# Kernel tuning notes

Hardware: AMD Instinct MI355X
Metric: run time of the kernel (lower is better)

Reference implementation:

```python
import jax, jax.numpy as jnp
import numpy as np

GROUP = 16  # quantization group size along in_features
EPS = 1e-5


def _qlora_linear(x, qw, sc, b, la, lb):
    # qw: [O, I] int4 codes; sc: [O, I//GROUP] fp32 group scales
    O, I = qw.shape
    w = (qw.astype(jnp.float32).reshape(O, I // GROUP, GROUP) * sc[:, :, None]).reshape(O, I)
    base = x @ w.T + b                      # [N, O]
    lora = (x @ la.T) @ lb.T                # [N, R] @ [R, O]
    return base + lora


def _layernorm(x, g, b):
    m = jnp.mean(x, axis=-1, keepdims=True)
    v = jnp.var(x, axis=-1, keepdims=True)
    return (x - m) * jax.lax.rsqrt(v + EPS) * g + b


def setup_inputs() -> dict:
    key = jax.random.key(0)
    ks = jax.random.split(key, 8)
    N, D, R, L = 16384, 1024, 32, 18  # tokens, BIGNET_DIM, lora_dim, num linears
    x = jax.random.normal(ks[0], (N, D), jnp.float32)
    qw = jax.random.randint(ks[1], (L, D, D), -8, 8, jnp.int32)  # signed 4-bit codes
    scales = jax.random.uniform(ks[2], (L, D, D // GROUP), jnp.float32, 0.005, 0.02)
    bias = 0.01 * jax.random.normal(ks[3], (L, D), jnp.float32)
    la = 0.001 * jax.random.normal(ks[4], (L, R, D), jnp.float32)
    lb = 0.01 * jax.random.normal(ks[5], (L, D, R), jnp.float32)
    ln_g = jnp.ones((5, D), jnp.float32) + 0.1 * jax.random.normal(ks[6], (5, D), jnp.float32)
    ln_b = 0.01 * jax.random.normal(ks[7], (5, D), jnp.float32)
    return {"x": x, "qw": qw, "scales": scales, "bias": bias,
            "la": la, "lb": lb, "ln_g": ln_g, "ln_b": ln_b}


def reference(x, qw, scales, bias, la, lb, ln_g, ln_b):
    h = x
    for blk in range(6):
        y = h
        for j in range(3):
            i = blk * 3 + j
            y = _qlora_linear(y, qw[i], scales[i], bias[i], la[i], lb[i])
            if j < 2:
                y = jax.nn.relu(y)
        h = y + h  # residual
        if blk < 5:
            h = _layernorm(h, ln_g[blk], ln_b[blk])
    return h
```

## Files before the change

### kernel.cpp

```cpp
#include <hip/hip_runtime.h>

#define DIM 1024
#define NTOK 16384

typedef __attribute__((ext_vector_type(8))) _Float16 f16x8;
typedef __attribute__((ext_vector_type(4))) _Float16 f16x4;
typedef __attribute__((ext_vector_type(4))) float f32x4;

__device__ __forceinline__ void gload_lds16(const void* g, void* l) {
  __builtin_amdgcn_global_load_lds(
      (const __attribute__((address_space(1))) void*)g,
      (__attribute__((address_space(3))) void*)l, 16, 0, 0);
}

__device__ __forceinline__ f16x8 ldsr(const char* smem, int byteoff) {
  return *(const f16x8*)(smem + byteoff);
}

__device__ __forceinline__ f32x4 mfma16(f16x8 a, f16x8 b, f32x4 c) {
  return __builtin_amdgcn_mfma_f32_16x16x32_f16(a, b, c, 0, 0, 0);
}

__global__ __launch_bounds__(256) void cvt_kernel(const float* __restrict__ in,
                                                  _Float16* __restrict__ out) {
  const int i = blockIdx.x * 256 + threadIdx.x;
  float4 v = reinterpret_cast<const float4*>(in)[i];
  f16x4 o;
  o[0] = (_Float16)v.x;
  o[1] = (_Float16)v.y;
  o[2] = (_Float16)v.z;
  o[3] = (_Float16)v.w;
  *reinterpret_cast<f16x4*>(&out[(size_t)i * 4]) = o;
}

__global__ __launch_bounds__(256) void build_weff(const int* __restrict__ qw,
                                                  const float* __restrict__ scales,
                                                  const float* __restrict__ la,
                                                  const float* __restrict__ lb,
                                                  _Float16* __restrict__ W) {
  __shared__ float la_s[32][256];
  __shared__ float lb_s[32][32];
  const int kt = blockIdx.x;
  const int ot = blockIdx.y;
  const int l = blockIdx.z;
  const int tid = threadIdx.x;

  for (int idx = tid; idx < 2048; idx += 256) {
    const int r = idx >> 6, c4 = (idx & 63) * 4;
    *(float4*)&la_s[r][c4] =
        *(const float4*)&la[((size_t)l * 32 + r) * DIM + kt * 256 + c4];
  }
  {
    const int o = tid >> 3, r4 = (tid & 7) * 4;
    *(float4*)&lb_s[o][r4] =
        *(const float4*)&lb[((size_t)l * DIM + ot * 32 + o) * 32 + r4];
  }
  __syncthreads();

  const int kq = tid & 63;
  const int os = tid >> 6;
  const int k0 = kq * 4;
  const int kg = kt * 256 + k0;
  const size_t rb = (size_t)l * DIM + ot * 32 + os * 8;

  int4 q[8];
  float sc[8];
#pragma unroll
  for (int oi = 0; oi < 8; ++oi) {
    q[oi] = *(const int4*)&qw[(rb + oi) * DIM + kg];
    sc[oi] = scales[(rb + oi) * 64 + (kg >> 4)];
  }

  float acc[8][4];
#pragma unroll
  for (int a = 0; a < 8; ++a)
#pragma unroll
    for (int b = 0; b < 4; ++b) acc[a][b] = 0.f;

#pragma unroll
  for (int r4 = 0; r4 < 8; ++r4) {
    float lbr[8][4];
#pragma unroll
    for (int oi = 0; oi < 8; ++oi) {
      const float4 v = *(const float4*)&lb_s[os * 8 + oi][r4 * 4];
      lbr[oi][0] = v.x;
      lbr[oi][1] = v.y;
      lbr[oi][2] = v.z;
      lbr[oi][3] = v.w;
    }
#pragma unroll
    for (int rr = 0; rr < 4; ++rr) {
      const float4 a4 = *(const float4*)&la_s[r4 * 4 + rr][k0];
#pragma unroll
      for (int oi = 0; oi < 8; ++oi) {
        acc[oi][0] = fmaf(lbr[oi][rr], a4.x, acc[oi][0]);
        acc[oi][1] = fmaf(lbr[oi][rr], a4.y, acc[oi][1]);
        acc[oi][2] = fmaf(lbr[oi][rr], a4.z, acc[oi][2]);
        acc[oi][3] = fmaf(lbr[oi][rr], a4.w, acc[oi][3]);
      }
    }
  }

#pragma unroll
  for (int oi = 0; oi < 8; ++oi) {
    f16x4 o4;
    o4[0] = (_Float16)(fmaf((float)q[oi].x, sc[oi], acc[oi][0]));
    o4[1] = (_Float16)(fmaf((float)q[oi].y, sc[oi], acc[oi][1]));
    o4[2] = (_Float16)(fmaf((float)q[oi].z, sc[oi], acc[oi][2]));
    o4[3] = (_Float16)(fmaf((float)q[oi].w, sc[oi], acc[oi][3]));
    *(f16x4*)&W[(rb + oi) * DIM + kg] = o4;
  }
}

#define ST_NONE ((void)0)
#define VM_NONE ((void)0)
#define VM4 asm volatile("s_waitcnt vmcnt(4)" ::: "memory")
#define VM0 asm volatile("s_waitcnt vmcnt(0)" ::: "memory")

#define RDA(BUF, FM, KS) \
  ldsr(smem, (((BUF)*2 + wm) << 14) + (((FM)*16 + r16) << 7) + (cks ^ ((KS) << 6)))
#define RDB(BUF, FN, KS)                                                        \
  ldsr(smem, 65536 + (((BUF)*2 + (wn >> 1)) << 14) +                            \
                 ((((wn & 1) * 64) + (FN)*16 + r16) << 7) + (cks ^ ((KS) << 6)))

#define PH(QQ, BUFC, STAGE, VMASM)                                          \
  {                                                                         \
    if ((QQ) == 0) {                                                        \
      _Pragma("unroll") for (int fn = 0; fn < 4; ++fn) {                    \
        bf[fn][0] = RDB(BUFC, fn, 0);                                       \
        bf[fn][1] = RDB(BUFC, fn, 1);                                       \
      }                                                                     \
    }                                                                       \
    f16x8 a00 = RDA(BUFC, 2 * (QQ), 0);                                     \
    f16x8 a01 = RDA(BUFC, 2 * (QQ), 1);                                     \
    f16x8 a10 = RDA(BUFC, 2 * (QQ) + 1, 0);                                 \
    f16x8 a11 = RDA(BUFC, 2 * (QQ) + 1, 1);                                 \
    STAGE;                                                                  \
    asm volatile("" ::: "memory");                                          \
    __builtin_amdgcn_s_barrier();                                           \
    asm volatile("s_waitcnt lgkmcnt(0)" ::: "memory");                      \
    __builtin_amdgcn_s_setprio(1);                                          \
    _Pragma("unroll") for (int fn = 0; fn < 4; ++fn) {                      \
      acc[2 * (QQ)][fn] = mfma16(bf[fn][0], a00, acc[2 * (QQ)][fn]);        \
      acc[2 * (QQ)][fn] = mfma16(bf[fn][1], a01, acc[2 * (QQ)][fn]);        \
      acc[2 * (QQ) + 1][fn] = mfma16(bf[fn][0], a10, acc[2 * (QQ) + 1][fn]); \
      acc[2 * (QQ) + 1][fn] = mfma16(bf[fn][1], a11, acc[2 * (QQ) + 1][fn]); \
    }                                                                       \
    __builtin_amdgcn_s_setprio(0);                                          \
    VMASM;                                                                  \
    asm volatile("" ::: "memory");                                          \
    __builtin_amdgcn_s_barrier();                                           \
  }

template <int MODE>
__global__ __launch_bounds__(512, 2) void qgemm(const _Float16* __restrict__ X,
                                                const _Float16* __restrict__ W,
                                                const float* __restrict__ bias,
                                                const _Float16* __restrict__ RES,
                                                void* __restrict__ OUT) {
  extern __shared__ char smem[];

  const int tid = threadIdx.x;
  const int wave = tid >> 6;
  const int lane = tid & 63;
  const int wm = wave >> 2;
  const int wn = wave & 3;
  const int bn = blockIdx.x;
  const int bm = blockIdx.y;

  const int r16 = lane & 15;
  const int cks = ((lane >> 4) * 16) ^ ((lane & 7) << 4);

  const int srl = lane >> 3;
  const int scs = ((lane & 7) ^ srl) << 3;

  f32x4 acc[8][4];
#pragma unroll
  for (int i = 0; i < 8; ++i)
#pragma unroll
    for (int j = 0; j < 4; ++j)
#pragma unroll
      for (int r = 0; r < 4; ++r) acc[i][j][r] = 0.f;

  auto stageA = [&](int buf, int h, int t) {
    const _Float16* g =
        X + (size_t)(bm * 256 + h * 128 + wave * 16 + srl) * DIM + t * 64 + scs;
    char* d = smem + (((buf * 2 + h) << 14) + wave * 2048);
    gload_lds16(g, d);
    gload_lds16(g + 8 * DIM, d + 1024);
  };
  auto stageB = [&](int buf, int h, int t) {
    const _Float16* g =
        W + (size_t)(bn * 256 + h * 128 + wave * 16 + srl) * DIM + t * 64 + scs;
    char* d = smem + (65536 + ((buf * 2 + h) << 14) + wave * 2048);
    gload_lds16(g, d);
    gload_lds16(g + 8 * DIM, d + 1024);
  };

  stageA(0, 0, 0);
  stageA(0, 1, 0);
  stageB(0, 0, 0);
  stageB(0, 1, 0);
  stageB(1, 0, 1);
  stageB(1, 1, 1);
  VM4;
  __builtin_amdgcn_s_barrier();

  f16x8 bf[4][2];

  for (int i = 0; i < 7; ++i) {
    const int t0 = 2 * i, t1 = 2 * i + 1;
    PH(0, 0, stageA(1, 0, t1), VM_NONE)
    PH(1, 0, stageA(1, 1, t1), VM_NONE)
    PH(2, 0, stageB(0, 0, t0 + 2), VM_NONE)
    PH(3, 0, stageB(0, 1, t0 + 2), VM4)
    PH(0, 1, stageA(0, 0, t0 + 2), VM_NONE)
    PH(1, 1, stageA(0, 1, t0 + 2), VM_NONE)
    PH(2, 1, stageB(1, 0, t1 + 2), VM_NONE)
    PH(3, 1, stageB(1, 1, t1 + 2), VM4)
  }
  PH(0, 0, stageA(1, 0, 15), VM_NONE)
  PH(1, 0, stageA(1, 1, 15), VM_NONE)
  PH(2, 0, ST_NONE, VM_NONE)
  PH(3, 0, ST_NONE, VM0)
  PH(0, 1, ST_NONE, VM_NONE)
  PH(1, 1, ST_NONE, VM_NONE)
  PH(2, 1, ST_NONE, VM_NONE)
  PH(3, 1, ST_NONE, VM_NONE)

  const int m_base = bm * 256 + wm * 128 + r16;
  const int o_base = bn * 256 + wn * 64 + (lane >> 4) * 4;
  float4 bv4[4];
#pragma unroll
  for (int fn = 0; fn < 4; ++fn)
    bv4[fn] = *(const float4*)&bias[o_base + fn * 16];

#pragma unroll
  for (int fm = 0; fm < 8; ++fm) {
    const size_t rowoff = (size_t)(m_base + fm * 16) * DIM;
#pragma unroll
    for (int fn = 0; fn < 4; ++fn) {
      const int o = o_base + fn * 16;
      float v0 = acc[fm][fn][0] + bv4[fn].x;
      float v1 = acc[fm][fn][1] + bv4[fn].y;
      float v2 = acc[fm][fn][2] + bv4[fn].z;
      float v3 = acc[fm][fn][3] + bv4[fn].w;
      if (MODE == 0) {
        f16x4 s;
        s[0] = (_Float16)fmaxf(v0, 0.f);
        s[1] = (_Float16)fmaxf(v1, 0.f);
        s[2] = (_Float16)fmaxf(v2, 0.f);
        s[3] = (_Float16)fmaxf(v3, 0.f);
        *(f16x4*)&((_Float16*)OUT)[rowoff + o] = s;
      } else {
        const f16x4 rv = *(const f16x4*)&RES[rowoff + o];
        v0 += (float)rv[0];
        v1 += (float)rv[1];
        v2 += (float)rv[2];
        v3 += (float)rv[3];
        if (MODE == 1) {
          f16x4 s;
          s[0] = (_Float16)v0;
          s[1] = (_Float16)v1;
          s[2] = (_Float16)v2;
          s[3] = (_Float16)v3;
          *(f16x4*)&((_Float16*)OUT)[rowoff + o] = s;
        } else {
          float4 s = {v0, v1, v2, v3};
          *(float4*)&((float*)OUT)[rowoff + o] = s;
        }
      }
    }
  }
}

__global__ __launch_bounds__(256) void ln_kernel(const _Float16* __restrict__ in,
                                                 const float* __restrict__ g,
                                                 const float* __restrict__ b,
                                                 _Float16* __restrict__ out) {
  const int row = blockIdx.x;
  const int tid = threadIdx.x;
  const _Float16* rp = in + (size_t)row * DIM;

  f16x4 raw = reinterpret_cast<const f16x4*>(rp)[tid];
  float v0 = (float)raw[0], v1 = (float)raw[1], v2 = (float)raw[2], v3 = (float)raw[3];
  float s = v0 + v1 + v2 + v3;
  float sq = v0 * v0 + v1 * v1 + v2 * v2 + v3 * v3;
#pragma unroll
  for (int off = 32; off > 0; off >>= 1) {
    s += __shfl_down(s, off);
    sq += __shfl_down(sq, off);
  }
  __shared__ float ss[4], sq4[4];
  if ((tid & 63) == 0) {
    ss[tid >> 6] = s;
    sq4[tid >> 6] = sq;
  }
  __syncthreads();
  s = ss[0] + ss[1] + ss[2] + ss[3];
  sq = sq4[0] + sq4[1] + sq4[2] + sq4[3];
  const float mean = s * (1.f / DIM);
  const float var = sq * (1.f / DIM) - mean * mean;
  const float inv = rsqrtf(var + 1e-5f);

  float4 gv = reinterpret_cast<const float4*>(g)[tid];
  float4 bv = reinterpret_cast<const float4*>(b)[tid];
  f16x4 o;
  o[0] = (_Float16)((v0 - mean) * inv * gv.x + bv.x);
  o[1] = (_Float16)((v1 - mean) * inv * gv.y + bv.y);
  o[2] = (_Float16)((v2 - mean) * inv * gv.z + bv.z);
  o[3] = (_Float16)((v3 - mean) * inv * gv.w + bv.w);
  *reinterpret_cast<f16x4*>(&out[(size_t)row * DIM + tid * 4]) = o;
}


extern "C" void kernel_launch(void* const* d_in, const int* in_sizes, int n_in,
                              void* d_out, int out_size, void* d_ws, size_t ws_size,
                              hipStream_t stream) {
  const float* x = (const float*)d_in[0];
  const int* qw = (const int*)d_in[1];
  const float* scales = (const float*)d_in[2];
  const float* bias = (const float*)d_in[3];
  const float* la = (const float*)d_in[4];
  const float* lb = (const float*)d_in[5];
  const float* ln_g = (const float*)d_in[6];
  const float* ln_b = (const float*)d_in[7];

  char* ws = (char*)d_ws;
  const size_t WEFF_BYTES = (size_t)18 * DIM * DIM * 2;
  const size_t ACT_BYTES = (size_t)NTOK * DIM * 2;
  _Float16* Weff = (_Float16*)ws;
  _Float16* bufA = (_Float16*)(ws + WEFF_BYTES);
  _Float16* bufB = (_Float16*)(ws + WEFF_BYTES + ACT_BYTES);
  _Float16* bufC = (_Float16*)(ws + WEFF_BYTES + 2 * ACT_BYTES);

  const int LDS_BYTES = 131072;
  (void)hipFuncSetAttribute((const void*)&qgemm<0>,
                            hipFuncAttributeMaxDynamicSharedMemorySize, LDS_BYTES);
  (void)hipFuncSetAttribute((const void*)&qgemm<1>,
                            hipFuncAttributeMaxDynamicSharedMemorySize, LDS_BYTES);
  (void)hipFuncSetAttribute((const void*)&qgemm<2>,
                            hipFuncAttributeMaxDynamicSharedMemorySize, LDS_BYTES);

  cvt_kernel<<<NTOK * DIM / 1024, 256, 0, stream>>>(x, bufA);
  build_weff<<<dim3(4, 32, 18), 256, 0, stream>>>(qw, scales, la, lb, Weff);

  const dim3 ggrid(DIM / 256, NTOK / 256);
  for (int blk = 0; blk < 6; ++blk) {
    const int i0 = blk * 3;
    const size_t wstep = (size_t)DIM * DIM;
    qgemm<0><<<ggrid, 512, LDS_BYTES, stream>>>(bufA, Weff + (size_t)i0 * wstep,
                                                bias + i0 * DIM, nullptr, bufB);
    qgemm<0><<<ggrid, 512, LDS_BYTES, stream>>>(bufB, Weff + (size_t)(i0 + 1) * wstep,
                                                bias + (i0 + 1) * DIM, nullptr, bufC);
    if (blk < 5) {
      qgemm<1><<<ggrid, 512, LDS_BYTES, stream>>>(bufC, Weff + (size_t)(i0 + 2) * wstep,
                                                  bias + (i0 + 2) * DIM, bufA, bufB);
      ln_kernel<<<NTOK, 256, 0, stream>>>(bufB, ln_g + blk * DIM, ln_b + blk * DIM, bufA);
    } else {
      qgemm<2><<<ggrid, 512, LDS_BYTES, stream>>>(bufC, Weff + (size_t)(i0 + 2) * wstep,
                                                  bias + (i0 + 2) * DIM, bufA, d_out);
    }
  }
}
```

Measured before the change: 869.8 us.

## Load weight fragments directly to registers, stage only activations through LDS

```diff
diff --git a/kernel.cpp b/kernel.cpp
--- a/kernel.cpp
+++ b/kernel.cpp
@@ -112,53 +112,13 @@
   }
 }
 
-#define ST_NONE ((void)0)
-#define VM_NONE ((void)0)
-#define VM4 asm volatile("s_waitcnt vmcnt(4)" ::: "memory")
-#define VM0 asm volatile("s_waitcnt vmcnt(0)" ::: "memory")
-
-#define RDA(BUF, FM, KS) \
-  ldsr(smem, (((BUF)*2 + wm) << 14) + (((FM)*16 + r16) << 7) + (cks ^ ((KS) << 6)))
-#define RDB(BUF, FN, KS)                                                        \
-  ldsr(smem, 65536 + (((BUF)*2 + (wn >> 1)) << 14) +                            \
-                 ((((wn & 1) * 64) + (FN)*16 + r16) << 7) + (cks ^ ((KS) << 6)))
-
-#define PH(QQ, BUFC, STAGE, VMASM)                                          \
-  {                                                                         \
-    if ((QQ) == 0) {                                                        \
-      _Pragma("unroll") for (int fn = 0; fn < 4; ++fn) {                    \
-        bf[fn][0] = RDB(BUFC, fn, 0);                                       \
-        bf[fn][1] = RDB(BUFC, fn, 1);                                       \
-      }                                                                     \
-    }                                                                       \
-    f16x8 a00 = RDA(BUFC, 2 * (QQ), 0);                                     \
-    f16x8 a01 = RDA(BUFC, 2 * (QQ), 1);                                     \
-    f16x8 a10 = RDA(BUFC, 2 * (QQ) + 1, 0);                                 \
-    f16x8 a11 = RDA(BUFC, 2 * (QQ) + 1, 1);                                 \
-    STAGE;                                                                  \
-    asm volatile("" ::: "memory");                                          \
-    __builtin_amdgcn_s_barrier();                                           \
-    asm volatile("s_waitcnt lgkmcnt(0)" ::: "memory");                      \
-    __builtin_amdgcn_s_setprio(1);                                          \
-    _Pragma("unroll") for (int fn = 0; fn < 4; ++fn) {                      \
-      acc[2 * (QQ)][fn] = mfma16(bf[fn][0], a00, acc[2 * (QQ)][fn]);        \
-      acc[2 * (QQ)][fn] = mfma16(bf[fn][1], a01, acc[2 * (QQ)][fn]);        \
-      acc[2 * (QQ) + 1][fn] = mfma16(bf[fn][0], a10, acc[2 * (QQ) + 1][fn]); \
-      acc[2 * (QQ) + 1][fn] = mfma16(bf[fn][1], a11, acc[2 * (QQ) + 1][fn]); \
-    }                                                                       \
-    __builtin_amdgcn_s_setprio(0);                                          \
-    VMASM;                                                                  \
-    asm volatile("" ::: "memory");                                          \
-    __builtin_amdgcn_s_barrier();                                           \
-  }
-
 template <int MODE>
 __global__ __launch_bounds__(512, 2) void qgemm(const _Float16* __restrict__ X,
                                                 const _Float16* __restrict__ W,
                                                 const float* __restrict__ bias,
                                                 const _Float16* __restrict__ RES,
                                                 void* __restrict__ OUT) {
-  extern __shared__ char smem[];
+  __shared__ char smem[65536];
 
   const int tid = threadIdx.x;
   const int wave = tid >> 6;
@@ -169,7 +129,8 @@
   const int bm = blockIdx.y;
 
   const int r16 = lane & 15;
-  const int cks = ((lane >> 4) * 16) ^ ((lane & 7) << 4);
+  const int koff = lane >> 4;
+  const int cks = (koff * 16) ^ ((lane & 7) << 4);
 
   const int srl = lane >> 3;
   const int scs = ((lane & 7) ^ srl) << 3;
@@ -182,58 +143,68 @@
 #pragma unroll
       for (int r = 0; r < 4; ++r) acc[i][j][r] = 0.f;
 
-  auto stageA = [&](int buf, int h, int t) {
+  auto stageA = [&](int buf, int t) {
     const _Float16* g =
-        X + (size_t)(bm * 256 + h * 128 + wave * 16 + srl) * DIM + t * 64 + scs;
-    char* d = smem + (((buf * 2 + h) << 14) + wave * 2048);
+        X + (size_t)(bm * 256 + wave * 16 + srl) * DIM + t * 64 + scs;
+    char* d = smem + (buf << 15) + wave * 2048;
     gload_lds16(g, d);
     gload_lds16(g + 8 * DIM, d + 1024);
+    gload_lds16(g + 128 * DIM, d + 16384);
+    gload_lds16(g + 136 * DIM, d + 16384 + 1024);
   };
-  auto stageB = [&](int buf, int h, int t) {
-    const _Float16* g =
-        W + (size_t)(bn * 256 + h * 128 + wave * 16 + srl) * DIM + t * 64 + scs;
-    char* d = smem + (65536 + ((buf * 2 + h) << 14) + wave * 2048);
-    gload_lds16(g, d);
-    gload_lds16(g + 8 * DIM, d + 1024);
+
+  const _Float16* Wb = W + (size_t)(bn * 256 + wn * 64 + r16) * DIM + koff * 8;
+  auto loadB = [&](f16x8(&b)[4][2], int t) {
+#pragma unroll
+    for (int fn = 0; fn < 4; ++fn)
+#pragma unroll
+      for (int ks = 0; ks < 2; ++ks)
+        b[fn][ks] = *(const f16x8*)(Wb + (size_t)fn * 16 * DIM + t * 64 + ks * 32);
   };
 
-  stageA(0, 0, 0);
-  stageA(0, 1, 0);
-  stageB(0, 0, 0);
-  stageB(0, 1, 0);
-  stageB(1, 0, 1);
-  stageB(1, 1, 1);
-  VM4;
-  __builtin_amdgcn_s_barrier();
-
-  f16x8 bf[4][2];
-
-  for (int i = 0; i < 7; ++i) {
-    const int t0 = 2 * i, t1 = 2 * i + 1;
-    PH(0, 0, stageA(1, 0, t1), VM_NONE)
-    PH(1, 0, stageA(1, 1, t1), VM_NONE)
-    PH(2, 0, stageB(0, 0, t0 + 2), VM_NONE)
-    PH(3, 0, stageB(0, 1, t0 + 2), VM4)
-    PH(0, 1, stageA(0, 0, t0 + 2), VM_NONE)
-    PH(1, 1, stageA(0, 1, t0 + 2), VM_NONE)
-    PH(2, 1, stageB(1, 0, t1 + 2), VM_NONE)
-    PH(3, 1, stageB(1, 1, t1 + 2), VM4)
-  }
-  PH(0, 0, stageA(1, 0, 15), VM_NONE)
-  PH(1, 0, stageA(1, 1, 15), VM_NONE)
-  PH(2, 0, ST_NONE, VM_NONE)
-  PH(3, 0, ST_NONE, VM0)
-  PH(0, 1, ST_NONE, VM_NONE)
-  PH(1, 1, ST_NONE, VM_NONE)
-  PH(2, 1, ST_NONE, VM_NONE)
-  PH(3, 1, ST_NONE, VM_NONE)
+  f16x8 b0[4][2], b1[4][2];
+
+  stageA(0, 0);
+  loadB(b0, 0);
+
+#define TILE(T, BCUR, BNEXT)                                                 \
+  {                                                                          \
+    asm volatile("s_waitcnt vmcnt(0)" ::: "memory");                         \
+    __builtin_amdgcn_s_barrier();                                            \
+    if ((T) + 1 < 16) {                                                      \
+      stageA(((T) + 1) & 1, (T) + 1);                                        \
+      loadB(BNEXT, (T) + 1);                                                 \
+    }                                                                        \
+    const int bufo = ((T)&1) << 15;                                          \
+    __builtin_amdgcn_s_setprio(1);                                           \
+    _Pragma("unroll") for (int q = 0; q < 4; ++q) {                          \
+      const int ra0 = bufo + ((wm * 128 + (2 * q) * 16 + r16) << 7);         \
+      const int ra1 = bufo + ((wm * 128 + (2 * q + 1) * 16 + r16) << 7);     \
+      f16x8 a00 = ldsr(smem, ra0 + cks);                                     \
+      f16x8 a01 = ldsr(smem, ra0 + (cks ^ 64));                              \
+      f16x8 a10 = ldsr(smem, ra1 + cks);                                     \
+      f16x8 a11 = ldsr(smem, ra1 + (cks ^ 64));                              \
+      _Pragma("unroll") for (int fn = 0; fn < 4; ++fn) {                     \
+        acc[2 * q][fn] = mfma16(BCUR[fn][0], a00, acc[2 * q][fn]);           \
+        acc[2 * q][fn] = mfma16(BCUR[fn][1], a01, acc[2 * q][fn]);           \
+        acc[2 * q + 1][fn] = mfma16(BCUR[fn][0], a10, acc[2 * q + 1][fn]);   \
+        acc[2 * q + 1][fn] = mfma16(BCUR[fn][1], a11, acc[2 * q + 1][fn]);   \
+      }                                                                      \
+    }                                                                        \
+    __builtin_amdgcn_s_setprio(0);                                           \
+  }
+
+  for (int t = 0; t < 16; t += 2) {
+    TILE(t, b0, b1)
+    TILE(t + 1, b1, b0)
+  }
+#undef TILE
 
   const int m_base = bm * 256 + wm * 128 + r16;
   const int o_base = bn * 256 + wn * 64 + (lane >> 4) * 4;
   float4 bv4[4];
 #pragma unroll
-  for (int fn = 0; fn < 4; ++fn)
-    bv4[fn] = *(const float4*)&bias[o_base + fn * 16];
+  for (int fn = 0; fn < 4; ++fn) bv4[fn] = *(const float4*)&bias[o_base + fn * 16];
 
 #pragma unroll
   for (int fm = 0; fm < 8; ++fm) {
@@ -334,14 +305,6 @@
   _Float16* bufB = (_Float16*)(ws + WEFF_BYTES + ACT_BYTES);
   _Float16* bufC = (_Float16*)(ws + WEFF_BYTES + 2 * ACT_BYTES);
 
-  const int LDS_BYTES = 131072;
-  (void)hipFuncSetAttribute((const void*)&qgemm<0>,
-                            hipFuncAttributeMaxDynamicSharedMemorySize, LDS_BYTES);
-  (void)hipFuncSetAttribute((const void*)&qgemm<1>,
-                            hipFuncAttributeMaxDynamicSharedMemorySize, LDS_BYTES);
-  (void)hipFuncSetAttribute((const void*)&qgemm<2>,
-                            hipFuncAttributeMaxDynamicSharedMemorySize, LDS_BYTES);
-
   cvt_kernel<<<NTOK * DIM / 1024, 256, 0, stream>>>(x, bufA);
   build_weff<<<dim3(4, 32, 18), 256, 0, stream>>>(qw, scales, la, lb, Weff);
 
@@ -349,17 +312,17 @@
   for (int blk = 0; blk < 6; ++blk) {
     const int i0 = blk * 3;
     const size_t wstep = (size_t)DIM * DIM;
-    qgemm<0><<<ggrid, 512, LDS_BYTES, stream>>>(bufA, Weff + (size_t)i0 * wstep,
-                                                bias + i0 * DIM, nullptr, bufB);
-    qgemm<0><<<ggrid, 512, LDS_BYTES, stream>>>(bufB, Weff + (size_t)(i0 + 1) * wstep,
-                                                bias + (i0 + 1) * DIM, nullptr, bufC);
+    qgemm<0><<<ggrid, 512, 0, stream>>>(bufA, Weff + (size_t)i0 * wstep,
+                                        bias + i0 * DIM, nullptr, bufB);
+    qgemm<0><<<ggrid, 512, 0, stream>>>(bufB, Weff + (size_t)(i0 + 1) * wstep,
+                                        bias + (i0 + 1) * DIM, nullptr, bufC);
     if (blk < 5) {
-      qgemm<1><<<ggrid, 512, LDS_BYTES, stream>>>(bufC, Weff + (size_t)(i0 + 2) * wstep,
-                                                  bias + (i0 + 2) * DIM, bufA, bufB);
+      qgemm<1><<<ggrid, 512, 0, stream>>>(bufC, Weff + (size_t)(i0 + 2) * wstep,
+                                          bias + (i0 + 2) * DIM, bufA, bufB);
       ln_kernel<<<NTOK, 256, 0, stream>>>(bufB, ln_g + blk * DIM, ln_b + blk * DIM, bufA);
     } else {
-      qgemm<2><<<ggrid, 512, LDS_BYTES, stream>>>(bufC, Weff + (size_t)(i0 + 2) * wstep,
-                                                  bias + (i0 + 2) * DIM, bufA, d_out);
+      qgemm<2><<<ggrid, 512, 0, stream>>>(bufC, Weff + (size_t)(i0 + 2) * wstep,
+                                          bias + (i0 + 2) * DIM, bufA, d_out);
     }
   }
 }
```

Result: slower. 1.193 ms (+37.2%).

## Stage GEMM epilogue through swizzled LDS for coalesced 16-byte global stores

Applied to the files above, without the earlier changes.

```diff
diff --git a/kernel.cpp b/kernel.cpp
--- a/kernel.cpp
+++ b/kernel.cpp
@@ -136,6 +136,7 @@
     f16x8 a10 = RDA(BUFC, 2 * (QQ) + 1, 0);                                 \
     f16x8 a11 = RDA(BUFC, 2 * (QQ) + 1, 1);                                 \
     STAGE;                                                                  \
+    if ((QQ) == 0) asm volatile("s_waitcnt lgkmcnt(8)" ::: "memory");       \
     asm volatile("" ::: "memory");                                          \
     __builtin_amdgcn_s_barrier();                                           \
     asm volatile("s_waitcnt lgkmcnt(0)" ::: "memory");                      \
@@ -228,47 +229,68 @@
   PH(2, 1, ST_NONE, VM_NONE)
   PH(3, 1, ST_NONE, VM_NONE)
 
-  const int m_base = bm * 256 + wm * 128 + r16;
-  const int o_base = bn * 256 + wn * 64 + (lane >> 4) * 4;
+  const int cq = (lane >> 4) * 4;
+  const int o_base = bn * 256 + wn * 64 + cq;
   float4 bv4[4];
 #pragma unroll
-  for (int fn = 0; fn < 4; ++fn)
-    bv4[fn] = *(const float4*)&bias[o_base + fn * 16];
+  for (int fn = 0; fn < 4; ++fn) bv4[fn] = *(const float4*)&bias[o_base + fn * 16];
 
 #pragma unroll
   for (int fm = 0; fm < 8; ++fm) {
-    const size_t rowoff = (size_t)(m_base + fm * 16) * DIM;
+    const int row = wm * 128 + fm * 16 + r16;
+    const int rx = (row & 7) << 4;
 #pragma unroll
     for (int fn = 0; fn < 4; ++fn) {
-      const int o = o_base + fn * 16;
+      const int colb = (wn * 64 + fn * 16 + cq) * 2;
+      const int addr = row * 512 + (((colb >> 4) << 4) ^ rx) + (colb & 15);
       float v0 = acc[fm][fn][0] + bv4[fn].x;
       float v1 = acc[fm][fn][1] + bv4[fn].y;
       float v2 = acc[fm][fn][2] + bv4[fn].z;
       float v3 = acc[fm][fn][3] + bv4[fn].w;
       if (MODE == 0) {
-        f16x4 s;
-        s[0] = (_Float16)fmaxf(v0, 0.f);
-        s[1] = (_Float16)fmaxf(v1, 0.f);
-        s[2] = (_Float16)fmaxf(v2, 0.f);
-        s[3] = (_Float16)fmaxf(v3, 0.f);
-        *(f16x4*)&((_Float16*)OUT)[rowoff + o] = s;
+        v0 = fmaxf(v0, 0.f);
+        v1 = fmaxf(v1, 0.f);
+        v2 = fmaxf(v2, 0.f);
+        v3 = fmaxf(v3, 0.f);
+      }
+      f16x4 h;
+      h[0] = (_Float16)v0;
+      h[1] = (_Float16)v1;
+      h[2] = (_Float16)v2;
+      h[3] = (_Float16)v3;
+      *(f16x4*)(smem + addr) = h;
+    }
+  }
+  __syncthreads();
+
+#pragma unroll
+  for (int i = 0; i < 16; ++i) {
+    const int idx = i * 512 + tid;
+    const int row = idx >> 5;
+    const int gb = idx & 31;
+    const f16x8 v = *(const f16x8*)(smem + row * 512 + ((gb ^ (row & 7)) << 4));
+    const size_t goff = (size_t)(bm * 256 + row) * DIM + bn * 256 + gb * 8;
+    if (MODE == 0) {
+      *(f16x8*)&((_Float16*)OUT)[goff] = v;
+    } else {
+      const f16x8 rv = *(const f16x8*)&RES[goff];
+      if (MODE == 1) {
+        f16x8 s;
+#pragma unroll
+        for (int e = 0; e < 8; ++e) s[e] = (_Float16)((float)v[e] + (float)rv[e]);
+        *(f16x8*)&((_Float16*)OUT)[goff] = s;
       } else {
-        const f16x4 rv = *(const f16x4*)&RES[rowoff + o];
-        v0 += (float)rv[0];
-        v1 += (float)rv[1];
-        v2 += (float)rv[2];
-        v3 += (float)rv[3];
-        if (MODE == 1) {
-          f16x4 s;
-          s[0] = (_Float16)v0;
-          s[1] = (_Float16)v1;
-          s[2] = (_Float16)v2;
-          s[3] = (_Float16)v3;
-          *(f16x4*)&((_Float16*)OUT)[rowoff + o] = s;
-        } else {
-          float4 s = {v0, v1, v2, v3};
-          *(float4*)&((float*)OUT)[rowoff + o] = s;
-        }
+        float4 s0, s1;
+        s0.x = (float)v[0] + (float)rv[0];
+        s0.y = (float)v[1] + (float)rv[1];
+        s0.z = (float)v[2] + (float)rv[2];
+        s0.w = (float)v[3] + (float)rv[3];
+        s1.x = (float)v[4] + (float)rv[4];
+        s1.y = (float)v[5] + (float)rv[5];
+        s1.z = (float)v[6] + (float)rv[6];
+        s1.w = (float)v[7] + (float)rv[7];
+        *(float4*)&((float*)OUT)[goff] = s0;
+        *(float4*)&((float*)OUT)[goff + 4] = s1;
       }
     }
   }
```

New measurement: 814.6 us. -6.4%, faster.
